# Kernel tuning notes

Hardware: AMD Instinct MI355X
Metric: run time of the kernel (lower is better)

The kernel has to match this reference:

```python
import jax, jax.numpy as jnp
import numpy as np

N = 20000      # nodes per type
E = 320000     # edges per relation
F = 512        # raw feature dim
H = 4          # attention heads
C = 128        # hidden_channels per head
B = 64         # batch_size (num graphs)
HH = H * C
INNER = 64
NEG_SLOPE = 0.2


def _gatv2(x_src, x_dst, ei, Wl, Wr, att, b):
    """PyG GATv2Conv (concat=True, add_self_loops=True, neg_slope=0.2).
    x_src:[Ns,Fin] x_dst:[Nd,Fin'] ei:[2,E] Wl,Wr:[Fin,H*C] att:[H,C] b:[H*C].
    Returns [Nd, H*C]. Self-loop edges appended (inputs assumed loop-free)."""
    n_dst = x_dst.shape[0]
    loop = jnp.arange(min(x_src.shape[0], n_dst), dtype=ei.dtype)
    src = jnp.concatenate([ei[0], loop])
    dst = jnp.concatenate([ei[1], loop])
    xl = (x_src @ Wl).reshape(-1, H, C)   # source-side transform
    xr = (x_dst @ Wr).reshape(-1, H, C)   # target-side transform
    e = jax.nn.leaky_relu(xl[src] + xr[dst], NEG_SLOPE)   # [E',H,C]
    logit = jnp.einsum('ehc,hc->eh', e, att)               # [E',H]
    m = jax.ops.segment_max(logit, dst, num_segments=n_dst)
    m = jnp.where(jnp.isfinite(m), m, 0.0)
    p = jnp.exp(logit - m[dst])
    s = jax.ops.segment_sum(p, dst, num_segments=n_dst)
    alpha = p / jnp.maximum(s[dst], 1e-16)                 # per-dst softmax
    out = jax.ops.segment_sum(alpha[:, :, None] * xl[src], dst, num_segments=n_dst)
    return out.reshape(n_dst, HH) + b


def _layer(x_i, x_j, ei_ii, ei_jj, ei_ij, ei_ji, Wl, Wr, att, b):
    # relation order: 0:(x_i->x_i) 1:(x_j->x_j) 2:(x_i->x_j) 3:(x_j->x_i); HeteroConv aggr='sum'
    oi = _gatv2(x_i, x_i, ei_ii, Wl[0], Wr[0], att[0], b[0]) \
       + _gatv2(x_j, x_i, ei_ji, Wl[3], Wr[3], att[3], b[3])
    oj = _gatv2(x_j, x_j, ei_jj, Wl[1], Wr[1], att[1], b[1]) \
       + _gatv2(x_i, x_j, ei_ij, Wl[2], Wr[2], att[2], b[2])
    # head-sum + tanh: x.view(-1, heads, hidden).sum(1).tanh()
    oi = jnp.tanh(oi.reshape(-1, H, C).sum(axis=1))
    oj = jnp.tanh(oj.reshape(-1, H, C).sum(axis=1))
    return oi, oj


def setup_inputs() -> dict:
    key = jax.random.key(0)
    ks = jax.random.split(key, 24)
    inp = {
        'x_i': jax.random.normal(ks[0], (N, F), jnp.float32),
        'x_j': jax.random.normal(ks[1], (N, F), jnp.float32),
        'ei_ii': jax.random.randint(ks[2], (2, E), 0, N, jnp.int32),
        'ei_jj': jax.random.randint(ks[3], (2, E), 0, N, jnp.int32),
        'ei_ij': jax.random.randint(ks[4], (2, E), 0, N, jnp.int32),
        'ei_ji': jax.random.randint(ks[5], (2, E), 0, N, jnp.int32),
        'batch_i': jnp.sort(jax.random.randint(ks[6], (N,), 0, B, jnp.int32)),
        'batch_j': jnp.sort(jax.random.randint(ks[7], (N,), 0, B, jnp.int32)),
        'Wl0': jax.random.normal(ks[8], (4, F, HH), jnp.float32) / np.sqrt(F),
        'Wr0': jax.random.normal(ks[9], (4, F, HH), jnp.float32) / np.sqrt(F),
        'att0': jax.random.normal(ks[10], (4, H, C), jnp.float32) / np.sqrt(C),
        'b0': jnp.zeros((4, HH), jnp.float32),
        'Wl1': jax.random.normal(ks[11], (4, C, HH), jnp.float32) / np.sqrt(C),
        'Wr1': jax.random.normal(ks[12], (4, C, HH), jnp.float32) / np.sqrt(C),
        'att1': jax.random.normal(ks[13], (4, H, C), jnp.float32) / np.sqrt(C),
        'b1': jnp.zeros((4, HH), jnp.float32),
        'W_out': jax.random.normal(ks[14], (C, 1), jnp.float32) / np.sqrt(C),
        'b_out': jnp.zeros((1,), jnp.float32),
        'W_i': jax.random.normal(ks[15], (C, INNER), jnp.float32) / np.sqrt(C),
        'b_i': jnp.zeros((INNER,), jnp.float32),
        'W_j': jax.random.normal(ks[16], (C, INNER), jnp.float32) / np.sqrt(C),
        'b_j': jnp.zeros((INNER,), jnp.float32),
    }
    return inp


def reference(x_i, x_j, ei_ii, ei_jj, ei_ij, ei_ji, batch_i, batch_j,
              Wl0, Wr0, att0, b0, Wl1, Wr1, att1, b1,
              W_out, b_out, W_i, b_i, W_j, b_j):
    x_i, x_j = _layer(x_i, x_j, ei_ii, ei_jj, ei_ij, ei_ji, Wl0, Wr0, att0, b0)
    x_i, x_j = _layer(x_i, x_j, ei_ii, ei_jj, ei_ij, ei_ji, Wl1, Wr1, att1, b1)
    # global_add_pool per graph, then unsqueeze(1) + tanh
    p_i = jnp.tanh(jax.ops.segment_sum(x_i, batch_i, num_segments=B))[:, None, :]  # [B,1,C]
    p_j = jnp.tanh(jax.ops.segment_sum(x_j, batch_j, num_segments=B))[:, None, :]
    y_i = p_i @ W_i + b_i   # [B,1,INNER]
    y_j = p_j @ W_j + b_j
    x = (p_i + p_j)[:, 0, :]            # cat along dim=1 then sum(dim=1)
    logits = jax.nn.sigmoid(x @ W_out + b_out)   # [B,1]
    return (logits, y_i, y_j)
```

## Files before the change

kernel.cpp:

```cpp
#include <hip/hip_runtime.h>

#define NN      20000
#define EE      320000
#define ETOT    340000
#define FD      512
#define HH_     4
#define CD      128
#define HHD     512
#define BG      64
#define INNERD  64

typedef __attribute__((ext_vector_type(8))) short bf16x8;
typedef __attribute__((ext_vector_type(4))) float f32x4;

__device__ __forceinline__ float bf2f(unsigned v) { return __uint_as_float(v << 16); }
__device__ __forceinline__ unsigned short f2bf(float f) {
    unsigned u = __float_as_uint(f);
    unsigned r = 0x7fffu + ((u >> 16) & 1u);
    return (unsigned short)((u + r) >> 16);
}
__device__ __forceinline__ void load8bf(const unsigned short* p, float* f) {
    uint4 u = *reinterpret_cast<const uint4*>(p);
    f[0] = bf2f(u.x & 0xffffu); f[1] = bf2f(u.x >> 16);
    f[2] = bf2f(u.y & 0xffffu); f[3] = bf2f(u.y >> 16);
    f[4] = bf2f(u.z & 0xffffu); f[5] = bf2f(u.z >> 16);
// ... 56 lines not shown
    if (idx < EE) { src = ei[idx]; dst = ei[EE + idx]; }
    else          { src = dst = idx - EE; }
    int pos = atomicAdd(&cursor[dst], 1);
    srcs[pos] = (unsigned short)src;
}

__global__ __launch_bounds__(256) void csr_hist4(
    const int* __restrict__ e0, const int* __restrict__ e1,
    const int* __restrict__ e2, const int* __restrict__ e3,
    int* __restrict__ cnt)
{
    int idx = blockIdx.x * blockDim.x + threadIdx.x;
    if (idx >= 4 * EE) return;
    int r = idx / EE, e = idx - r * EE;
    const int* ei = r == 0 ? e0 : r == 1 ? e1 : r == 2 ? e2 : e3;
    atomicAdd(&cnt[r * NN + ei[EE + e]], 1);
}

__global__ __launch_bounds__(1024) void csr_scan4(const int* __restrict__ cnt_all,
                                                  int* __restrict__ rowptr_all,
                                                  int* __restrict__ cursor_all)
{
    const int r = blockIdx.x;
    const int* cnt = cnt_all + r * NN;
    int* rowptr = rowptr_all + r * (NN + 4);
    int* cursor = cursor_all + r * NN;
    __shared__ int part[1024];
    int t = threadIdx.x;
    int base = t * 20;
    int s = 0;
    #pragma unroll
    for (int i = 0; i < 20; ++i) { int n = base + i; if (n < NN) s += cnt[n] + 1; }
    part[t] = s;
    __syncthreads();
    for (int off = 1; off < 1024; off <<= 1) {
        int v = (t >= off) ? part[t - off] : 0;
        __syncthreads();
        part[t] += v;
        __syncthreads();
    }
    int run = (t > 0) ? part[t - 1] : 0;
    #pragma unroll
    for (int i = 0; i < 20; ++i) {
        int n = base + i;
        if (n < NN) { rowptr[n] = run; cursor[n] = run; run += cnt[n] + 1; }
    }
    if (t == 1023) rowptr[NN] = run;
}

__global__ __launch_bounds__(256) void csr_scatter4(
    const int* __restrict__ e0, const int* __restrict__ e1,
    const int* __restrict__ e2, const int* __restrict__ e3,
    int* __restrict__ cursor_all, unsigned short* __restrict__ srcs_all)
{
    int idx = blockIdx.x * blockDim.x + threadIdx.x;
    if (idx >= 4 * ETOT) return;
    int r = idx / ETOT, t = idx - r * ETOT;
    const int* ei = r == 0 ? e0 : r == 1 ? e1 : r == 2 ? e2 : e3;
    int src, dst;
    if (t < EE) { src = ei[t]; dst = ei[EE + t]; }
    else        { src = dst = t - EE; }
    int pos = atomicAdd(&cursor_all[r * NN + dst], 1);
    srcs_all[(size_t)r * ETOT + pos] = (unsigned short)src;
}

__device__ __forceinline__ void wsplit_body(const float* __restrict__ W,
                                            unsigned short* __restrict__ Whi,
                                            unsigned short* __restrict__ Wlo,
                                            int K, int bid)
{
    __shared__ float tile[64][65];
    const int nt = 512 / 64;
    int in = bid % nt; int ik = (bid / nt) % (K / 64); int r = bid / (nt * (K / 64));
    int t = threadIdx.x;
    const float* Wr_ = W + (size_t)r * K * 512;
    #pragma unroll
    for (int rep = 0; rep < 16; ++rep) {
// ... 407 lines not shown
    if (k < e) {
        int s0 = sr[k];
        float A0[8];
        load8bf(xl + (size_t)s0 * HHD + lane * 8, A0);
        float d0 = quad_reduce(edge_logit(A0, br, ta));
        float p0 = __expf(d0);
        den += p0;
        #pragma unroll
        for (int j = 0; j < 8; ++j) n[j] += p0 * A0[j];
    }
}

__device__ __forceinline__ void gat_rel(
    const int* __restrict__ rp, const unsigned short* __restrict__ sr,
    const unsigned short* __restrict__ xl, const unsigned short* __restrict__ xr,
    const float* __restrict__ att, int dst, int lane, float* o)
{
    int beg = rp[dst], end = rp[dst + 1];
    float br[8], ta[8];
    load8bf(xr + (size_t)dst * HHD + lane * 8, br);
    #pragma unroll
    for (int j = 0; j < 8; ++j) ta[j] = att[lane * 8 + j];
    float n[8] = {}; float den = 0.f;
    gat_drain(sr, xl, br, ta, beg, end, n, den, lane);
    float inv = 1.f / den;
    #pragma unroll
    for (int j = 0; j < 8; ++j) {
        o[j] = n[j] * inv;
        o[j] += __shfl_xor(o[j], 16);
        o[j] += __shfl_xor(o[j], 32);
    }
}

__device__ __forceinline__ void gat_rel2(
    const int* __restrict__ rp0, const unsigned short* __restrict__ sr0,
    const unsigned short* __restrict__ xl0, const unsigned short* __restrict__ xr0,
    const float* __restrict__ attA,
    const int* __restrict__ rp1, const unsigned short* __restrict__ sr1,
    const unsigned short* __restrict__ xl1, const unsigned short* __restrict__ xr1,
    const float* __restrict__ attB,
    int dst, int lane, float* o0, float* o1)
{
    int k0 = rp0[dst], e0 = rp0[dst + 1];
    int k1 = rp1[dst], e1 = rp1[dst + 1];
    float br0[8], br1[8], ta0[8], ta1[8];
    load8bf(xr0 + (size_t)dst * HHD + lane * 8, br0);
    load8bf(xr1 + (size_t)dst * HHD + lane * 8, br1);
    #pragma unroll
    for (int j = 0; j < 8; ++j) { ta0[j] = attA[lane * 8 + j]; ta1[j] = attB[lane * 8 + j]; }

    float n0[8] = {}, n1[8] = {};
    float den0 = 0.f, den1 = 0.f;

    while (k0 + 2 <= e0 && k1 + 2 <= e1) {
        int sa0 = sr0[k0], sa1 = sr0[k0 + 1];
        int sb0 = sr1[k1], sb1 = sr1[k1 + 1];
        float A0[8], A1[8], B0[8], B1[8];
        load8bf(xl0 + (size_t)sa0 * HHD + lane * 8, A0);
        load8bf(xl0 + (size_t)sa1 * HHD + lane * 8, A1);
// ... 23 lines not shown
    gat_drain(sr1, xl1, br1, ta1, k1, e1, n1, den1, lane);

    float i0 = 1.f / den0, i1 = 1.f / den1;
    #pragma unroll
    for (int j = 0; j < 8; ++j) {
        o0[j] = n0[j] * i0;
        o0[j] += __shfl_xor(o0[j], 16);
        o0[j] += __shfl_xor(o0[j], 32);
        o1[j] = n1[j] * i1;
        o1[j] += __shfl_xor(o1[j], 16);
        o1[j] += __shfl_xor(o1[j], 32);
    }
}

__device__ __forceinline__ void aggr4d_body(
    int dst, int lane,
    const int* __restrict__ rp0, const unsigned short* __restrict__ sr0,
    const unsigned short* __restrict__ xl0, const unsigned short* __restrict__ xr0,
    const float* __restrict__ attA,
    const int* __restrict__ rp1, const unsigned short* __restrict__ sr1,
    const unsigned short* __restrict__ xl1, const unsigned short* __restrict__ xr1,
    const float* __restrict__ attB,
    float* __restrict__ acc, int fin_mode,
    const float* __restrict__ bA, const float* __restrict__ bB,
    unsigned short* __restrict__ z)
{
    float o0[8], o1[8];
    gat_rel2(rp0, sr0, xl0, xr0, attA, rp1, sr1, xl1, xr1, attB, dst, lane, o0, o1);
    #pragma unroll
    for (int j = 0; j < 8; ++j) o1[j] += o0[j];

    if (lane < 16) {
        size_t ai = (size_t)dst * CD + lane * 8;
        int c0 = lane * 8;
        #pragma unroll
        for (int j = 0; j < 8; ++j) {
            float bb = 0.f;
            #pragma unroll
            for (int h = 0; h < HH_; ++h)
                bb += bA[h * CD + c0 + j] + bB[h * CD + c0 + j];
            o1[j] = tanhf(o1[j] + bb);
        }
        if (fin_mode == 1) {
            #pragma unroll
            for (int j = 0; j < 8; ++j) z[ai + j] = f2bf(o1[j]);
        } else {
            #pragma unroll
            for (int j = 0; j < 8; ++j) acc[ai + j] = o1[j];
        }
    }
}

__global__ __launch_bounds__(256) void fused_aggr4(
    const int* __restrict__ rowptr, const unsigned short* __restrict__ srcs,
    const unsigned short* __restrict__ xl, const unsigned short* __restrict__ xr,
    const float* __restrict__ att,
    float* __restrict__ acc, int add_in, int fin_mode,
    const float* __restrict__ bA, const float* __restrict__ bB,
    unsigned short* __restrict__ z,
    const int* __restrict__ batch, float* __restrict__ pool)
{
    int dst = (int)((blockIdx.x * (size_t)blockDim.x + threadIdx.x) >> 6);
    int lane = threadIdx.x & 63;
    if (dst >= NN) return;

    float o[8];
    gat_rel(rowptr, srcs, xl, xr, att, dst, lane, o);

    if (lane < 16) {
        size_t ai = (size_t)dst * CD + lane * 8;
        if (add_in) {
            #pragma unroll
            for (int j = 0; j < 8; ++j) o[j] += acc[ai + j];
        }
        if (fin_mode == 0) {
            #pragma unroll
            for (int j = 0; j < 8; ++j) acc[ai + j] = o[j];
        } else {
            int c0 = lane * 8;
            #pragma unroll
            for (int j = 0; j < 8; ++j) {
                float bb = 0.f;
// ... 8 lines not shown
            } else {
                #pragma unroll
                for (int j = 0; j < 8; ++j) acc[ai + j] = o[j];
            }
        }
    }
}

__global__ __launch_bounds__(256) void fused_aggr4d(
    const int* __restrict__ rp0, const unsigned short* __restrict__ sr0,
    const unsigned short* __restrict__ xl0, const unsigned short* __restrict__ xr0,
    const float* __restrict__ attA,
    const int* __restrict__ rp1, const unsigned short* __restrict__ sr1,
    const unsigned short* __restrict__ xl1, const unsigned short* __restrict__ xr1,
    const float* __restrict__ attB,
    float* __restrict__ acc, int fin_mode,
    const float* __restrict__ bA, const float* __restrict__ bB,
    unsigned short* __restrict__ z,
    const int* __restrict__ batch, float* __restrict__ pool)
{
    int dst = (int)((blockIdx.x * (size_t)blockDim.x + threadIdx.x) >> 6);
    int lane = threadIdx.x & 63;
    if (dst >= NN) return;
    aggr4d_body(dst, lane, rp0, sr0, xl0, xr0, attA, rp1, sr1, xl1, xr1, attB,
                acc, fin_mode, bA, bB, z);
}

__global__ __launch_bounds__(256) void fused_aggr4d_pair(
    const int* __restrict__ irp0, const unsigned short* __restrict__ isr0,
    const unsigned short* __restrict__ ixl0, const unsigned short* __restrict__ ixr0,
    const float* __restrict__ iattA,
    const int* __restrict__ irp1, const unsigned short* __restrict__ isr1,
    const unsigned short* __restrict__ ixl1, const unsigned short* __restrict__ ixr1,
    const float* __restrict__ iattB,
    float* __restrict__ accA,
    const float* __restrict__ ibA, const float* __restrict__ ibB,
    const int* __restrict__ jrp0, const unsigned short* __restrict__ jsr0,
    const unsigned short* __restrict__ jxl0, const unsigned short* __restrict__ jxr0,
    const float* __restrict__ jattA,
    const int* __restrict__ jrp1, const unsigned short* __restrict__ jsr1,
    const unsigned short* __restrict__ jxl1, const unsigned short* __restrict__ jxr1,
    const float* __restrict__ jattB,
    float* __restrict__ accB,
    const float* __restrict__ jbA, const float* __restrict__ jbB)
{
    const int half = NN / 4;
    int lane = threadIdx.x & 63;
    if ((int)blockIdx.x < half) {
        int dst = (int)((blockIdx.x * (size_t)blockDim.x + threadIdx.x) >> 6);
        if (dst >= NN) return;
        aggr4d_body(dst, lane, irp0, isr0, ixl0, ixr0, iattA,
                    irp1, isr1, ixl1, ixr1, iattB, accA, 2, ibA, ibB, nullptr);
    } else {
        int dst = (int)(((blockIdx.x - half) * (size_t)blockDim.x + threadIdx.x) >> 6);
        if (dst >= NN) return;
        aggr4d_body(dst, lane, jrp0, jsr0, jxl0, jxr0, jattA,
                    jrp1, jsr1, jxl1, jxr1, jattB, accB, 2, jbA, jbB, nullptr);
    }
}

template <typename TA, bool A_EXACT>
__global__ __launch_bounds__(256, 3) void gemm_aggr_fused(
    int ngemm, int ntot,
    const TA* __restrict__ A0, const TA* __restrict__ A1,
    const TA* __restrict__ A2, const TA* __restrict__ A3,
    const unsigned short* __restrict__ B0h, const unsigned short* __restrict__ B0l,
    const unsigned short* __restrict__ B1h, const unsigned short* __restrict__ B1l,
    const unsigned short* __restrict__ B2h, const unsigned short* __restrict__ B2l,
    const unsigned short* __restrict__ B3h, const unsigned short* __restrict__ B3l,
    unsigned short* __restrict__ C0, unsigned short* __restrict__ C1,
    unsigned short* __restrict__ C2, unsigned short* __restrict__ C3,
    int M, int K, int N,
    const int* __restrict__ rp0, const unsigned short* __restrict__ sr0,
    const unsigned short* __restrict__ xl0, const unsigned short* __restrict__ xr0,
    const float* __restrict__ attA,
    const int* __restrict__ rp1, const unsigned short* __restrict__ sr1,
    const unsigned short* __restrict__ xl1, const unsigned short* __restrict__ xr1,
    const float* __restrict__ attB,
    float* __restrict__ acc, int fin_mode,
    const float* __restrict__ bA, const float* __restrict__ bB,
    unsigned short* __restrict__ zout)
{
    int b = (int)blockIdx.x;
    int cb = (int)(((long long)b * ngemm) / ntot);
    bool is_gemm = ((int)(((long long)(b + 1) * ngemm) / ntot) > cb);
    if (is_gemm) {
        int g = cb;
        int xcd = g & 7, q8 = ngemm >> 3, r8 = ngemm & 7;
        int work = (xcd < r8 ? xcd * (q8 + 1) : r8 * (q8 + 1) + (xcd - r8) * q8) + (g >> 3);
        const int gx = N / 128, gy = (M + 127) / 128;
        int bx = work % gx; int t2 = work / gx; int by = t2 % gy; int bz = t2 / gy;
        const TA* A = bz == 0 ? A0 : bz == 1 ? A1 : bz == 2 ? A2 : A3;
        const unsigned short* Bh = bz == 0 ? B0h : bz == 1 ? B1h : bz == 2 ? B2h : B3h;
        const unsigned short* Bl = bz == 0 ? B0l : bz == 1 ? B1l : bz == 2 ? B2l : B3l;
        unsigned short* C = bz == 0 ? C0 : bz == 1 ? C1 : bz == 2 ? C2 : C3;
        gemm_body<TA, A_EXACT>(A, Bh, Bl, C, bx, by, M, K, N);
    } else {
        int ab = b - cb;
        int dst = (int)(((size_t)ab * blockDim.x + threadIdx.x) >> 6);
        int lane = threadIdx.x & 63;
        if (dst >= NN) return;
        aggr4d_body(dst, lane, rp0, sr0, xl0, xr0, attA, rp1, sr1, xl1, xr1, attB,
                    acc, fin_mode, bA, bB, zout);
    }
}

__global__ __launch_bounds__(512) void pool_reduce(
    const float* __restrict__ acc, const int* __restrict__ batch,
    float* __restrict__ pool)
{
    int b = blockIdx.x;
    int t = threadIdx.x & (CD - 1);
    int q = threadIdx.x >> 7;
    int lo, hi;
    { int l = 0, r = NN; while (l < r) { int m = (l + r) >> 1; if (batch[m] < b) l = m + 1; else r = m; } lo = l; }
    { int l = lo, r = NN; while (l < r) { int m = (l + r) >> 1; if (batch[m] <= b) l = m + 1; else r = m; } hi = l; }
    float s = 0.f;
// ... 88 lines not shown
                            const float* att, const float* bias, int fin_mode,
                            unsigned short* zout, const int* batch, float* pool,
                            const Ws& w, hipStream_t stream)
{
    dim3 gg(HHD / 128, (NN + 127) / 128, 4);
    size_t off0 = (size_t)rids[0] * HHD * K;
    size_t off1 = (size_t)rids[1] * HHD * K;
    gemm_mfma_t4<TA, A_EXACT><<<gg, 256, 0, stream>>>(
        srcA[0], dstA[0], srcA[1], dstA[1],
        WTl_h + off0, WTl_l + off0, WTr_h + off0, WTr_l + off0,
        WTl_h + off1, WTl_l + off1, WTr_h + off1, WTr_l + off1,
        w.xl, w.xr, w.xl2, w.xr2, NN, K, HHD);
    fused_aggr4d<<<NN / 4, 256, 0, stream>>>(
        rp[0], sr[0], w.xl, w.xr, att + (size_t)rids[0] * HHD,
        rp[1], sr[1], w.xl2, w.xr2, att + (size_t)rids[1] * HHD,
        w.acc, fin_mode,
        bias + (size_t)rids[0] * HHD, bias + (size_t)rids[1] * HHD,
        zout, batch, pool);
}

template <typename TA, bool A_EXACT>
static void run_group_fat_t(const TA* srcA[2], const TA* dstA[2],
                            const int* rp[2], const unsigned short* sr[2],
                            const int rids[2], int K,
                            const unsigned short* WTl_h, const unsigned short* WTl_l,
                            const unsigned short* WTr_h, const unsigned short* WTr_l,
                            const float* att, const float* bias, int fin_mode,
                            unsigned short* zout, const int* batch, float* pool,
                            const Ws& w, hipStream_t stream)
{
    dim3 gg(HHD / 128, (NN + 127) / 128, 2);
    const int ablocks = NN / 4;
    for (int q = 0; q < 2; ++q) {
        int r = rids[q];
        size_t off = (size_t)r * HHD * K;
        gemm_mfma_t<TA, A_EXACT><<<gg, 256, 0, stream>>>(
            srcA[q], dstA[q],
            WTl_h + off, WTl_l + off, WTr_h + off, WTr_l + off,
            w.xl, w.xr, NN, K, HHD);
        int fm = (q == 1) ? fin_mode : 0;
        fused_aggr4<<<ablocks, 256, 0, stream>>>(
            rp[q], sr[q], w.xl, w.xr,
            att + (size_t)r * HHD,
            w.acc, q > 0 ? 1 : 0, fm,
            bias + (size_t)rids[0] * HHD, bias + (size_t)rids[1] * HHD,
            zout, batch, pool);
    }
}

template <typename TA, bool A_EXACT>
static void run_group_fat(const TA* srcA[2], const TA* dstA[2],
                          const int* rp[2], const unsigned short* sr[2],
                          const int rids[2], int K,
                          const float* Wl, const float* Wr, const float* att,
                          const float* bias, int fin_mode,
                          unsigned short* zout, const int* batch, float* pool,
                          const Ws& w, hipStream_t stream)
{
    dim3 gg(HHD / 64, (NN + 63) / 64, 2);
    const int ablocks = NN / 4;
    for (int q = 0; q < 2; ++q) {
        int r = rids[q];
        gemm_mfma<TA, A_EXACT><<<gg, 256, 0, stream>>>(
            srcA[q], dstA[q],
            Wl + (size_t)r * K * HHD, Wr + (size_t)r * K * HHD, HHD,
            w.xl, w.xr, NN, K, HHD);
        int fm = (q == 1) ? fin_mode : 0;
        fused_aggr4<<<ablocks, 256, 0, stream>>>(
            rp[q], sr[q], w.xl, w.xr,
            att + (size_t)r * HHD,
            w.acc, q > 0 ? 1 : 0, fm,
            bias + (size_t)rids[0] * HHD, bias + (size_t)rids[1] * HHD,
            zout, batch, pool);
    }
}

template <typename TA, bool A_EXACT>
static void run_group_thin(const TA* srcA[2], const TA* dstA[2],
                           const int* eis[2], const int rids[2], int K,
                           const float* Wl, const float* Wr, const float* att,
                           const float* bias, int fin_mode,
                           unsigned short* zout, const int* batch, float* pool,
                           const Ws& w, hipStream_t stream)
{
    dim3 gg(2, (NN + 63) / 64, 2);
    const int ablocks = NN / 4;
// ... 35 lines not shown
    const float* b0    = (const float*)d_in[11];
    const float* Wl1   = (const float*)d_in[12];
    const float* Wr1   = (const float*)d_in[13];
    const float* att1  = (const float*)d_in[14];
    const float* b1    = (const float*)d_in[15];
    const float* W_out = (const float*)d_in[16];
    const float* b_out = (const float*)d_in[17];
    const float* W_i   = (const float*)d_in[18];
    const float* b_i   = (const float*)d_in[19];
    const float* W_j   = (const float*)d_in[20];
    const float* b_j   = (const float*)d_in[21];
    float* out = (float*)d_out;

    const size_t FAT2_BYTES = (size_t)NN * HHD * 2 * 2 + (size_t)NN * CD * 4
                            + (size_t)NN * CD * 2 * 2 + 4 * (size_t)ETOT * 2
                            + 4 * (size_t)(NN + 4) * 4 + 4 * (size_t)NN * 4 * 2
                            + (size_t)BG * CD * 4 * 2;
    const size_t FAT1_BYTES = (size_t)NN * HHD * 2 * 2 + (size_t)NN * CD * 4
                            + (size_t)NN * CD * 2 * 2 + (size_t)ETOT * 2
                            + (size_t)(NN + 4) * 4 + (size_t)NN * 4 * 2
                            + (size_t)BG * CD * 4 * 2;
    const size_t WT0_ONE = (size_t)4 * 512 * 512 * 2;
    const size_t WT1_ONE = (size_t)4 * 512 * 128 * 2;
    const size_t WT_BYTES = 4 * WT0_ONE + 4 * WT1_ONE;
    const size_t X2_BYTES = 2 * (size_t)NN * HHD * 2;
    const size_t ACC2_BYTES = (size_t)NN * CD * 4;

    const int ncsr = (ws_size >= FAT2_BYTES) ? 4 : 1;
    const bool fat = (ws_size >= FAT1_BYTES);
    const bool fat_t = (ws_size >= FAT2_BYTES + WT_BYTES);
    const bool fat_m = (ws_size >= FAT2_BYTES + WT_BYTES + X2_BYTES);
    const bool fat_f = (ws_size >= FAT2_BYTES + WT_BYTES + 3 * X2_BYTES);
    const bool fat_g = (ws_size >= FAT2_BYTES + WT_BYTES + 3 * X2_BYTES + ACC2_BYTES);

    Ws w;
    char* p = (char*)d_ws;
    size_t xbytes = fat ? (size_t)NN * HHD * 2 : (size_t)NN * CD * 2;
    w.xl     = (unsigned short*)p; p += xbytes;
    w.xr     = (unsigned short*)p; p += xbytes;
    w.acc    = (float*)p;          p += (size_t)NN * CD * 4;
    w.z_i    = (unsigned short*)p; p += (size_t)NN * CD * 2;
    w.z_j    = (unsigned short*)p; p += (size_t)NN * CD * 2;
    {
        int* rowptr_all = (int*)p;            p += (size_t)ncsr * (NN + 4) * 4;
        unsigned short* srcs_all = (unsigned short*)p; p += (size_t)ncsr * ETOT * 2;
        for (int r = 0; r < 4; ++r) {
            int rr = (r < ncsr) ? r : 0;
            w.rowptr[r] = rowptr_all + (size_t)rr * (NN + 4);
            w.srcs[r]   = srcs_all + (size_t)rr * ETOT;
        }
    }
    w.cnt    = (int*)p;            p += (size_t)ncsr * NN * 4;
    w.cursor = (int*)p;            p += (size_t)ncsr * NN * 4;
    w.pool_i = (float*)p;          p += (size_t)BG * CD * 4;
    w.pool_j = (float*)p;          p += (size_t)BG * CD * 4;
    if (fat_t) {
        w.wt0l_h = (unsigned short*)p; p += WT0_ONE;
        w.wt0l_l = (unsigned short*)p; p += WT0_ONE;
        w.wt0r_h = (unsigned short*)p; p += WT0_ONE;
        w.wt0r_l = (unsigned short*)p; p += WT0_ONE;
        w.wt1l_h = (unsigned short*)p; p += WT1_ONE;
        w.wt1l_l = (unsigned short*)p; p += WT1_ONE;
        w.wt1r_h = (unsigned short*)p; p += WT1_ONE;
        w.wt1r_l = (unsigned short*)p; p += WT1_ONE;
    }
    if (fat_m) {
        w.xl2 = (unsigned short*)p; p += (size_t)NN * HHD * 2;
        w.xr2 = (unsigned short*)p; p += (size_t)NN * HHD * 2;
// ... 12 lines not shown
        hipMemsetAsync(w.pool_i, 0, (size_t)BG * CD * sizeof(float), stream);
        hipMemsetAsync(w.pool_j, 0, (size_t)BG * CD * sizeof(float), stream);
    }

    const int* eis_all[4] = { ei_ii, ei_jj, ei_ij, ei_ji };
    const float* srcA0_i[2] = { x_i, x_j };  const float* dstA0_i[2] = { x_i, x_i };
    const float* srcA0_j[2] = { x_j, x_i };  const float* dstA0_j[2] = { x_j, x_j };
    const int rids_i[2] = { 0, 3 };
    const int rids_j[2] = { 1, 2 };
    const unsigned short* srcA1_i[2] = { w.z_i, w.z_j };
    const unsigned short* dstA1_i[2] = { w.z_i, w.z_i };
    const unsigned short* srcA1_j[2] = { w.z_j, w.z_i };
    const unsigned short* dstA1_j[2] = { w.z_j, w.z_j };

    if (fat_t) {
        hipMemsetAsync(w.cnt, 0, 4 * NN * sizeof(int), stream);
        csr_hist4<<<(4 * EE + 255) / 256, 256, 0, stream>>>(
            ei_ii, ei_jj, ei_ij, ei_ji, w.cnt);
        csr_scan4<<<4, 1024, 0, stream>>>(w.cnt, w.rowptr[0], w.cursor);
        csr_scatter4<<<(4 * ETOT + 255) / 256, 256, 0, stream>>>(
            ei_ii, ei_jj, ei_ij, ei_ji, w.cursor, w.srcs[0]);
        wsplit_all<<<640, 256, 0, stream>>>(
            Wl0, Wr0, Wl1, Wr1,
            w.wt0l_h, w.wt0l_l, w.wt0r_h, w.wt0r_l,
            w.wt1l_h, w.wt1l_l, w.wt1r_h, w.wt1r_l);

        const int* rp_i[2] = { w.rowptr[0], w.rowptr[3] };
        const unsigned short* sr_i[2] = { w.srcs[0], w.srcs[3] };
        const int* rp_j[2] = { w.rowptr[1], w.rowptr[2] };
        const unsigned short* sr_j[2] = { w.srcs[1], w.srcs[2] };

        if (fat_g) {
            const size_t o0 = (size_t)0 * HHD * FD, o3 = (size_t)3 * HHD * FD;
            const size_t o1 = (size_t)1 * HHD * FD, o2 = (size_t)2 * HHD * FD;
            const size_t p0 = (size_t)0 * HHD * CD, p1 = (size_t)1 * HHD * CD;
            const size_t p2 = (size_t)2 * HHD * CD, p3 = (size_t)3 * HHD * CD;
            dim3 gg(HHD / 128, (NN + 127) / 128, 4);
            gemm_mfma_t4<float, false><<<gg, 256, 0, stream>>>(
                x_i, x_i, x_j, x_i,
                w.wt0l_h + o0, w.wt0l_l + o0, w.wt0r_h + o0, w.wt0r_l + o0,
                w.wt0l_h + o3, w.wt0l_l + o3, w.wt0r_h + o3, w.wt0r_l + o3,
                w.xl, w.xr, w.xl2, w.xr2, NN, FD, HHD);
            const int ngemm0 = (HHD / 128) * ((NN + 127) / 128) * 4;
            const int ntot0 = ngemm0 + NN / 4;
            gemm_aggr_fused<float, false><<<ntot0, 256, 0, stream>>>(
                ngemm0, ntot0,
                x_j, x_j, x_i, x_j,
                w.wt0l_h + o1, w.wt0l_l + o1, w.wt0r_h + o1, w.wt0r_l + o1,
                w.wt0l_h + o2, w.wt0l_l + o2, w.wt0r_h + o2, w.wt0r_l + o2,
                w.xl3, w.xr3, w.xl4, w.xr4, NN, FD, HHD,
                w.rowptr[0], w.srcs[0], w.xl, w.xr, att0 + (size_t)0 * HHD,
                w.rowptr[3], w.srcs[3], w.xl2, w.xr2, att0 + (size_t)3 * HHD,
                w.acc, 1, b0 + (size_t)0 * HHD, b0 + (size_t)3 * HHD, w.z_i);
            gemm_aggr_fused<unsigned short, true><<<ntot0, 256, 0, stream>>>(
                ngemm0, ntot0,
                w.z_i, w.z_i, w.z_i, w.z_i,
                w.wt1l_h + p0, w.wt1l_l + p0, w.wt1r_h + p0, w.wt1r_l + p0,
                w.wt1r_h + p3, w.wt1r_l + p3, w.wt1l_h + p2, w.wt1l_l + p2,
                w.xl, w.xr, w.xr2, w.xl2, NN, CD, HHD,
                w.rowptr[1], w.srcs[1], w.xl3, w.xr3, att0 + (size_t)1 * HHD,
                w.rowptr[2], w.srcs[2], w.xl4, w.xr4, att0 + (size_t)2 * HHD,
                w.acc, 1, b0 + (size_t)1 * HHD, b0 + (size_t)2 * HHD, w.z_j);
            gemm_mfma_t4<unsigned short, true><<<gg, 256, 0, stream>>>(
                w.z_j, w.z_j, w.z_j, w.z_j,
                w.wt1l_h + p3, w.wt1l_l + p3, w.wt1l_h + p1, w.wt1l_l + p1,
                w.wt1r_h + p1, w.wt1r_l + p1, w.wt1r_h + p2, w.wt1r_l + p2,
                w.xl4, w.xl3, w.xr3, w.xr4, NN, CD, HHD);
            fused_aggr4d_pair<<<2 * (NN / 4), 256, 0, stream>>>(
                w.rowptr[0], w.srcs[0], w.xl, w.xr, att1 + (size_t)0 * HHD,
                w.rowptr[3], w.srcs[3], w.xl4, w.xr2, att1 + (size_t)3 * HHD,
                w.acc, b1 + (size_t)0 * HHD, b1 + (size_t)3 * HHD,
                w.rowptr[1], w.srcs[1], w.xl3, w.xr3, att1 + (size_t)1 * HHD,
                w.rowptr[2], w.srcs[2], w.xl2, w.xr4, att1 + (size_t)2 * HHD,
                w.acc2, b1 + (size_t)1 * HHD, b1 + (size_t)2 * HHD);
            pool_reduce2<<<2 * BG, 512, 0, stream>>>(
                w.acc, batch_i, w.pool_i, w.acc2, batch_j, w.pool_j);
        } else if (fat_f) {
            const size_t o0 = (size_t)0 * HHD * FD, o3 = (size_t)3 * HHD * FD;
            const size_t o1 = (size_t)1 * HHD * FD, o2 = (size_t)2 * HHD * FD;
            dim3 gg(HHD / 128, (NN + 127) / 128, 4);
            gemm_mfma_t4<float, false><<<gg, 256, 0, stream>>>(
                x_i, x_i, x_j, x_i,
                w.wt0l_h + o0, w.wt0l_l + o0, w.wt0r_h + o0, w.wt0r_l + o0,
                w.wt0l_h + o3, w.wt0l_l + o3, w.wt0r_h + o3, w.wt0r_l + o3,
                w.xl, w.xr, w.xl2, w.xr2, NN, FD, HHD);
            const int ngemm = (HHD / 128) * ((NN + 127) / 128) * 4;
            const int ntot = ngemm + NN / 4;
            gemm_aggr_fused<float, false><<<ntot, 256, 0, stream>>>(
                ngemm, ntot,
                x_j, x_j, x_i, x_j,
                w.wt0l_h + o1, w.wt0l_l + o1, w.wt0r_h + o1, w.wt0r_l + o1,
                w.wt0l_h + o2, w.wt0l_l + o2, w.wt0r_h + o2, w.wt0r_l + o2,
                w.xl3, w.xr3, w.xl4, w.xr4, NN, FD, HHD,
                w.rowptr[0], w.srcs[0], w.xl, w.xr, att0 + (size_t)0 * HHD,
                w.rowptr[3], w.srcs[3], w.xl2, w.xr2, att0 + (size_t)3 * HHD,
                w.acc, 1, b0 + (size_t)0 * HHD, b0 + (size_t)3 * HHD, w.z_i);
            fused_aggr4d<<<NN / 4, 256, 0, stream>>>(
                w.rowptr[1], w.srcs[1], w.xl3, w.xr3, att0 + (size_t)1 * HHD,
                w.rowptr[2], w.srcs[2], w.xl4, w.xr4, att0 + (size_t)2 * HHD,
                w.acc, 1, b0 + (size_t)1 * HHD, b0 + (size_t)2 * HHD,
                w.z_j, nullptr, nullptr);
            dim3 g8(HHD / 128, (NN + 127) / 128, 8);
            gemm_mfma_L1x8<<<g8, 256, 0, stream>>>(
                w.z_i, w.z_j, w.wt1l_h, w.wt1l_l, w.wt1r_h, w.wt1r_l,
                w.xl, w.xr, w.xl2, w.xr2, w.xl3, w.xr3, w.xl4, w.xr4,
                NN, CD, HHD);
            fused_aggr4d<<<NN / 4, 256, 0, stream>>>(
                w.rowptr[0], w.srcs[0], w.xl, w.xr, att1 + (size_t)0 * HHD,
                w.rowptr[3], w.srcs[3], w.xl2, w.xr2, att1 + (size_t)3 * HHD,
                w.acc, 2, b1 + (size_t)0 * HHD, b1 + (size_t)3 * HHD,
                nullptr, nullptr, nullptr);
            pool_reduce<<<BG, 512, 0, stream>>>(w.acc, batch_i, w.pool_i);
            fused_aggr4d<<<NN / 4, 256, 0, stream>>>(
                w.rowptr[1], w.srcs[1], w.xl3, w.xr3, att1 + (size_t)1 * HHD,
                w.rowptr[2], w.srcs[2], w.xl4, w.xr4, att1 + (size_t)2 * HHD,
                w.acc, 2, b1 + (size_t)1 * HHD, b1 + (size_t)2 * HHD,
                nullptr, nullptr, nullptr);
            pool_reduce<<<BG, 512, 0, stream>>>(w.acc, batch_j, w.pool_j);
        } else if (fat_m) {
            run_group_fat_m<float, false>(srcA0_i, dstA0_i, rp_i, sr_i, rids_i, FD,
                                          w.wt0l_h, w.wt0l_l, w.wt0r_h, w.wt0r_l,
                                          att0, b0, 1, w.z_i, nullptr, nullptr, w, stream);
            run_group_fat_m<float, false>(srcA0_j, dstA0_j, rp_j, sr_j, rids_j, FD,
                                          w.wt0l_h, w.wt0l_l, w.wt0r_h, w.wt0r_l,
                                          att0, b0, 1, w.z_j, nullptr, nullptr, w, stream);
            run_group_fat_m<unsigned short, true>(srcA1_i, dstA1_i, rp_i, sr_i, rids_i, CD,
                                                  w.wt1l_h, w.wt1l_l, w.wt1r_h, w.wt1r_l,
                                                  att1, b1, 2, nullptr, batch_i, w.pool_i, w, stream);
            pool_reduce<<<BG, 512, 0, stream>>>(w.acc, batch_i, w.pool_i);
            run_group_fat_m<unsigned short, true>(srcA1_j, dstA1_j, rp_j, sr_j, rids_j, CD,
                                                  w.wt1l_h, w.wt1l_l, w.wt1r_h, w.wt1r_l,
// ... 36 lines not shown
        } else {
            for (int pass = 0; pass < 4; ++pass) {
                const int* rids = (pass & 1) ? rids_j : rids_i;
                for (int q = 0; q < 2; ++q) {
                    int r = rids[q];
                    build_csr(eis_all[r], w.rowptr[0], w.srcs[0], w.cnt, w.cursor, stream);
                    dim3 gg(HHD / 64, (NN + 63) / 64, 2);
                    if (pass < 2) {
                        const float* sa = (pass == 0) ? srcA0_i[q] : srcA0_j[q];
                        const float* da = (pass == 0) ? dstA0_i[q] : dstA0_j[q];
                        gemm_mfma<float, false><<<gg, 256, 0, stream>>>(
                            sa, da, Wl0 + (size_t)r * FD * HHD, Wr0 + (size_t)r * FD * HHD,
                            HHD, w.xl, w.xr, NN, FD, HHD);
                        fused_aggr4<<<NN / 4, 256, 0, stream>>>(
                            w.rowptr[0], w.srcs[0], w.xl, w.xr, att0 + (size_t)r * HHD,
                            w.acc, q, (q == 1) ? 1 : 0,
                            b0 + (size_t)rids[0] * HHD, b0 + (size_t)rids[1] * HHD,
                            (pass == 0) ? w.z_i : w.z_j, nullptr, nullptr);
                    } else {
                        const unsigned short* sa = (pass == 2) ? srcA1_i[q] : srcA1_j[q];
                        const unsigned short* da = (pass == 2) ? dstA1_i[q] : dstA1_j[q];
                        gemm_mfma<unsigned short, true><<<gg, 256, 0, stream>>>(
                            sa, da, Wl1 + (size_t)r * CD * HHD, Wr1 + (size_t)r * CD * HHD,
                            HHD, w.xl, w.xr, NN, CD, HHD);
                        fused_aggr4<<<NN / 4, 256, 0, stream>>>(
                            w.rowptr[0], w.srcs[0], w.xl, w.xr, att1 + (size_t)r * HHD,
                            w.acc, q, (q == 1) ? 2 : 0,
                            b1 + (size_t)rids[0] * HHD, b1 + (size_t)rids[1] * HHD,
                            nullptr, (pass == 2) ? batch_i : batch_j,
                            (pass == 2) ? w.pool_i : w.pool_j);
                    }
                }
                if (pass == 2)
                    pool_reduce<<<BG, 512, 0, stream>>>(w.acc, batch_i, w.pool_i);
                else if (pass == 3)
                    pool_reduce<<<BG, 512, 0, stream>>>(w.acc, batch_j, w.pool_j);
            }
        }
    } else {
        const int* eis_i[2] = { ei_ii, ei_ji };
        const int* eis_j[2] = { ei_jj, ei_ij };
        run_group_thin<float, false>(srcA0_i, dstA0_i, eis_i, rids_i, FD, Wl0, Wr0, att0, b0,
// ... 13 lines not shown
```

Before: 1.249 ms.

## Bucket CSR neighbor lists by source range for gather locality

CSR construction now keys each row on destination plus one of eight source-index buckets, so every destination's neighbor list comes out roughly sorted by source. Aggregation kernels read row bounds with a stride to span all buckets of a destination. The aim is more locality and cache reuse in the xl row gathers. In exchange it adds an 8x larger count, cursor and rowptr array and a heavier single-block scan. It also drops the proportional interleaving of GEMM and aggregation blocks in the fused kernel, putting all GEMM blocks first.

```diff
diff --git a/kernel.cpp b/kernel.cpp
--- a/kernel.cpp
+++ b/kernel.cpp
@@ -9,6 +9,8 @@
 #define HHD     512
 #define BG      64
 #define INNERD  64
+#define NBUCK   8
+#define BROWS   (NN * NBUCK)
 
 typedef __attribute__((ext_vector_type(8))) short bf16x8;
 typedef __attribute__((ext_vector_type(4))) float f32x4;
@@ -95,7 +97,8 @@
     if (idx >= 4 * EE) return;
     int r = idx / EE, e = idx - r * EE;
     const int* ei = r == 0 ? e0 : r == 1 ? e1 : r == 2 ? e2 : e3;
-    atomicAdd(&cnt[r * NN + ei[EE + e]], 1);
+    int src = ei[e], dst = ei[EE + e];
+    atomicAdd(&cnt[r * BROWS + dst * NBUCK + src / 2500], 1);
 }
 
 __global__ __launch_bounds__(1024) void csr_scan4(const int* __restrict__ cnt_all,
@@ -103,15 +106,21 @@
                                                   int* __restrict__ cursor_all)
 {
     const int r = blockIdx.x;
-    const int* cnt = cnt_all + r * NN;
-    int* rowptr = rowptr_all + r * (NN + 4);
-    int* cursor = cursor_all + r * NN;
+    const int* cnt = cnt_all + r * BROWS;
+    int* rowptr = rowptr_all + r * (BROWS + 4);
+    int* cursor = cursor_all + r * BROWS;
     __shared__ int part[1024];
     int t = threadIdx.x;
-    int base = t * 20;
+    const int RPT = (BROWS + 1023) / 1024;
+    int base = t * RPT;
     int s = 0;
-    #pragma unroll
-    for (int i = 0; i < 20; ++i) { int n = base + i; if (n < NN) s += cnt[n] + 1; }
+    for (int i = 0; i < RPT; ++i) {
+        int row = base + i;
+        if (row < BROWS) {
+            int dst = row >> 3, bu = row & 7;
+            s += cnt[row] + ((bu == dst / 2500) ? 1 : 0);
+        }
+    }
     part[t] = s;
     __syncthreads();
     for (int off = 1; off < 1024; off <<= 1) {
@@ -121,12 +130,15 @@
         __syncthreads();
     }
     int run = (t > 0) ? part[t - 1] : 0;
-    #pragma unroll
-    for (int i = 0; i < 20; ++i) {
-        int n = base + i;
-        if (n < NN) { rowptr[n] = run; cursor[n] = run; run += cnt[n] + 1; }
-    }
-    if (t == 1023) rowptr[NN] = run;
+    for (int i = 0; i < RPT; ++i) {
+        int row = base + i;
+        if (row < BROWS) {
+            int dst = row >> 3, bu = row & 7;
+            rowptr[row] = run; cursor[row] = run;
+            run += cnt[row] + ((bu == dst / 2500) ? 1 : 0);
+        }
+    }
+    if (t == 1023) rowptr[BROWS] = run;
 }
 
 __global__ __launch_bounds__(256) void csr_scatter4(
@@ -141,7 +153,8 @@
     int src, dst;
     if (t < EE) { src = ei[t]; dst = ei[EE + t]; }
     else        { src = dst = t - EE; }
-    int pos = atomicAdd(&cursor_all[r * NN + dst], 1);
+    int row = r * BROWS + dst * NBUCK + src / 2500;
+    int pos = atomicAdd(&cursor_all[row], 1);
     srcs_all[(size_t)r * ETOT + pos] = (unsigned short)src;
 }
 
@@ -579,9 +592,9 @@
 __device__ __forceinline__ void gat_rel(
     const int* __restrict__ rp, const unsigned short* __restrict__ sr,
     const unsigned short* __restrict__ xl, const unsigned short* __restrict__ xr,
-    const float* __restrict__ att, int dst, int lane, float* o)
-{
-    int beg = rp[dst], end = rp[dst + 1];
+    const float* __restrict__ att, int dst, int lane, int rs, float* o)
+{
+    int beg = rp[dst * rs], end = rp[dst * rs + rs];
     float br[8], ta[8];
     load8bf(xr + (size_t)dst * HHD + lane * 8, br);
     #pragma unroll
@@ -604,10 +617,10 @@
     const int* __restrict__ rp1, const unsigned short* __restrict__ sr1,
     const unsigned short* __restrict__ xl1, const unsigned short* __restrict__ xr1,
     const float* __restrict__ attB,
-    int dst, int lane, float* o0, float* o1)
-{
-    int k0 = rp0[dst], e0 = rp0[dst + 1];
-    int k1 = rp1[dst], e1 = rp1[dst + 1];
+    int dst, int lane, int rs, float* o0, float* o1)
+{
+    int k0 = rp0[dst * rs], e0 = rp0[dst * rs + rs];
+    int k1 = rp1[dst * rs], e1 = rp1[dst * rs + rs];
     float br0[8], br1[8], ta0[8], ta1[8];
     load8bf(xr0 + (size_t)dst * HHD + lane * 8, br0);
     load8bf(xr1 + (size_t)dst * HHD + lane * 8, br1);
@@ -661,7 +674,7 @@
 }
 
 __device__ __forceinline__ void aggr4d_body(
-    int dst, int lane,
+    int dst, int lane, int rs,
     const int* __restrict__ rp0, const unsigned short* __restrict__ sr0,
     const unsigned short* __restrict__ xl0, const unsigned short* __restrict__ xr0,
     const float* __restrict__ attA,
@@ -673,7 +686,7 @@
     unsigned short* __restrict__ z)
 {
     float o0[8], o1[8];
-    gat_rel2(rp0, sr0, xl0, xr0, attA, rp1, sr1, xl1, xr1, attB, dst, lane, o0, o1);
+    gat_rel2(rp0, sr0, xl0, xr0, attA, rp1, sr1, xl1, xr1, attB, dst, lane, rs, o0, o1);
     #pragma unroll
     for (int j = 0; j < 8; ++j) o1[j] += o0[j];
 
@@ -702,7 +715,7 @@
     const int* __restrict__ rowptr, const unsigned short* __restrict__ srcs,
     const unsigned short* __restrict__ xl, const unsigned short* __restrict__ xr,
     const float* __restrict__ att,
-    float* __restrict__ acc, int add_in, int fin_mode,
+    float* __restrict__ acc, int add_in, int fin_mode, int rs,
     const float* __restrict__ bA, const float* __restrict__ bB,
     unsigned short* __restrict__ z,
     const int* __restrict__ batch, float* __restrict__ pool)
@@ -712,7 +725,7 @@
     if (dst >= NN) return;
 
     float o[8];
-    gat_rel(rowptr, srcs, xl, xr, att, dst, lane, o);
+    gat_rel(rowptr, srcs, xl, xr, att, dst, lane, rs, o);
 
     if (lane < 16) {
         size_t ai = (size_t)dst * CD + lane * 8;
@@ -751,7 +764,7 @@
     const int* __restrict__ rp1, const unsigned short* __restrict__ sr1,
     const unsigned short* __restrict__ xl1, const unsigned short* __restrict__ xr1,
     const float* __restrict__ attB,
-    float* __restrict__ acc, int fin_mode,
+    float* __restrict__ acc, int fin_mode, int rs,
     const float* __restrict__ bA, const float* __restrict__ bB,
     unsigned short* __restrict__ z,
     const int* __restrict__ batch, float* __restrict__ pool)
@@ -759,11 +772,12 @@
     int dst = (int)((blockIdx.x * (size_t)blockDim.x + threadIdx.x) >> 6);
     int lane = threadIdx.x & 63;
     if (dst >= NN) return;
-    aggr4d_body(dst, lane, rp0, sr0, xl0, xr0, attA, rp1, sr1, xl1, xr1, attB,
+    aggr4d_body(dst, lane, rs, rp0, sr0, xl0, xr0, attA, rp1, sr1, xl1, xr1, attB,
                 acc, fin_mode, bA, bB, z);
 }
 
 __global__ __launch_bounds__(256) void fused_aggr4d_pair(
+    int rs,
     const int* __restrict__ irp0, const unsigned short* __restrict__ isr0,
     const unsigned short* __restrict__ ixl0, const unsigned short* __restrict__ ixr0,
     const float* __restrict__ iattA,
@@ -786,19 +800,19 @@
     if ((int)blockIdx.x < half) {
         int dst = (int)((blockIdx.x * (size_t)blockDim.x + threadIdx.x) >> 6);
         if (dst >= NN) return;
-        aggr4d_body(dst, lane, irp0, isr0, ixl0, ixr0, iattA,
+        aggr4d_body(dst, lane, rs, irp0, isr0, ixl0, ixr0, iattA,
                     irp1, isr1, ixl1, ixr1, iattB, accA, 2, ibA, ibB, nullptr);
     } else {
         int dst = (int)(((blockIdx.x - half) * (size_t)blockDim.x + threadIdx.x) >> 6);
         if (dst >= NN) return;
-        aggr4d_body(dst, lane, jrp0, jsr0, jxl0, jxr0, jattA,
+        aggr4d_body(dst, lane, rs, jrp0, jsr0, jxl0, jxr0, jattA,
                     jrp1, jsr1, jxl1, jxr1, jattB, accB, 2, jbA, jbB, nullptr);
     }
 }
 
 template <typename TA, bool A_EXACT>
 __global__ __launch_bounds__(256, 3) void gemm_aggr_fused(
-    int ngemm, int ntot,
+    int ngemm, int rs,
     const TA* __restrict__ A0, const TA* __restrict__ A1,
     const TA* __restrict__ A2, const TA* __restrict__ A3,
     const unsigned short* __restrict__ B0h, const unsigned short* __restrict__ B0l,
@@ -818,13 +832,10 @@
     const float* __restrict__ bA, const float* __restrict__ bB,
     unsigned short* __restrict__ zout)
 {
-    int b = (int)blockIdx.x;
-    int cb = (int)(((long long)b * ngemm) / ntot);
-    bool is_gemm = ((int)(((long long)(b + 1) * ngemm) / ntot) > cb);
-    if (is_gemm) {
-        int g = cb;
-        int xcd = g & 7, q8 = ngemm >> 3, r8 = ngemm & 7;
-        int work = (xcd < r8 ? xcd * (q8 + 1) : r8 * (q8 + 1) + (xcd - r8) * q8) + (g >> 3);
+    if ((int)blockIdx.x < ngemm) {
+        int b = blockIdx.x;
+        int xcd = b & 7, q8 = ngemm >> 3, r8 = ngemm & 7;
+        int work = (xcd < r8 ? xcd * (q8 + 1) : r8 * (q8 + 1) + (xcd - r8) * q8) + (b >> 3);
         const int gx = N / 128, gy = (M + 127) / 128;
         int bx = work % gx; int t2 = work / gx; int by = t2 % gy; int bz = t2 / gy;
         const TA* A = bz == 0 ? A0 : bz == 1 ? A1 : bz == 2 ? A2 : A3;
@@ -833,11 +844,10 @@
         unsigned short* C = bz == 0 ? C0 : bz == 1 ? C1 : bz == 2 ? C2 : C3;
         gemm_body<TA, A_EXACT>(A, Bh, Bl, C, bx, by, M, K, N);
     } else {
-        int ab = b - cb;
-        int dst = (int)(((size_t)ab * blockDim.x + threadIdx.x) >> 6);
+        int dst = (int)(((blockIdx.x - ngemm) * (size_t)blockDim.x + threadIdx.x) >> 6);
         int lane = threadIdx.x & 63;
         if (dst >= NN) return;
-        aggr4d_body(dst, lane, rp0, sr0, xl0, xr0, attA, rp1, sr1, xl1, xr1, attB,
+        aggr4d_body(dst, lane, rs, rp0, sr0, xl0, xr0, attA, rp1, sr1, xl1, xr1, attB,
                     acc, fin_mode, bA, bB, zout);
     }
 }
@@ -956,7 +966,7 @@
     fused_aggr4d<<<NN / 4, 256, 0, stream>>>(
         rp[0], sr[0], w.xl, w.xr, att + (size_t)rids[0] * HHD,
         rp[1], sr[1], w.xl2, w.xr2, att + (size_t)rids[1] * HHD,
-        w.acc, fin_mode,
+        w.acc, fin_mode, NBUCK,
         bias + (size_t)rids[0] * HHD, bias + (size_t)rids[1] * HHD,
         zout, batch, pool);
 }
@@ -984,7 +994,7 @@
         fused_aggr4<<<ablocks, 256, 0, stream>>>(
             rp[q], sr[q], w.xl, w.xr,
             att + (size_t)r * HHD,
-            w.acc, q > 0 ? 1 : 0, fm,
+            w.acc, q > 0 ? 1 : 0, fm, NBUCK,
             bias + (size_t)rids[0] * HHD, bias + (size_t)rids[1] * HHD,
             zout, batch, pool);
     }
@@ -1011,7 +1021,7 @@
         fused_aggr4<<<ablocks, 256, 0, stream>>>(
             rp[q], sr[q], w.xl, w.xr,
             att + (size_t)r * HHD,
-            w.acc, q > 0 ? 1 : 0, fm,
+            w.acc, q > 0 ? 1 : 0, fm, 1,
             bias + (size_t)rids[0] * HHD, bias + (size_t)rids[1] * HHD,
             zout, batch, pool);
     }
@@ -1077,7 +1087,7 @@
 
     const size_t FAT2_BYTES = (size_t)NN * HHD * 2 * 2 + (size_t)NN * CD * 4
                             + (size_t)NN * CD * 2 * 2 + 4 * (size_t)ETOT * 2
-                            + 4 * (size_t)(NN + 4) * 4 + 4 * (size_t)NN * 4 * 2
+                            + 4 * (size_t)(BROWS + 4) * 4 + 4 * (size_t)BROWS * 4 * 2
                             + (size_t)BG * CD * 4 * 2;
     const size_t FAT1_BYTES = (size_t)NN * HHD * 2 * 2 + (size_t)NN * CD * 4
                             + (size_t)NN * CD * 2 * 2 + (size_t)ETOT * 2
@@ -1105,16 +1115,16 @@
     w.z_i    = (unsigned short*)p; p += (size_t)NN * CD * 2;
     w.z_j    = (unsigned short*)p; p += (size_t)NN * CD * 2;
     {
-        int* rowptr_all = (int*)p;            p += (size_t)ncsr * (NN + 4) * 4;
+        int* rowptr_all = (int*)p;            p += (size_t)ncsr * (BROWS + 4) * 4;
         unsigned short* srcs_all = (unsigned short*)p; p += (size_t)ncsr * ETOT * 2;
         for (int r = 0; r < 4; ++r) {
             int rr = (r < ncsr) ? r : 0;
-            w.rowptr[r] = rowptr_all + (size_t)rr * (NN + 4);
+            w.rowptr[r] = rowptr_all + (size_t)rr * (BROWS + 4);
             w.srcs[r]   = srcs_all + (size_t)rr * ETOT;
         }
     }
-    w.cnt    = (int*)p;            p += (size_t)ncsr * NN * 4;
-    w.cursor = (int*)p;            p += (size_t)ncsr * NN * 4;
+    w.cnt    = (int*)p;            p += (size_t)ncsr * BROWS * 4;
+    w.cursor = (int*)p;            p += (size_t)ncsr * BROWS * 4;
     w.pool_i = (float*)p;          p += (size_t)BG * CD * 4;
     w.pool_j = (float*)p;          p += (size_t)BG * CD * 4;
     if (fat_t) {
@@ -1157,7 +1167,7 @@
     const unsigned short* dstA1_j[2] = { w.z_j, w.z_j };
 
     if (fat_t) {
-        hipMemsetAsync(w.cnt, 0, 4 * NN * sizeof(int), stream);
+        hipMemsetAsync(w.cnt, 0, 4 * (size_t)BROWS * sizeof(int), stream);
         csr_hist4<<<(4 * EE + 255) / 256, 256, 0, stream>>>(
             ei_ii, ei_jj, ei_ij, ei_ji, w.cnt);
         csr_scan4<<<4, 1024, 0, stream>>>(w.cnt, w.rowptr[0], w.cursor);
@@ -1185,9 +1195,8 @@
                 w.wt0l_h + o3, w.wt0l_l + o3, w.wt0r_h + o3, w.wt0r_l + o3,
                 w.xl, w.xr, w.xl2, w.xr2, NN, FD, HHD);
             const int ngemm0 = (HHD / 128) * ((NN + 127) / 128) * 4;
-            const int ntot0 = ngemm0 + NN / 4;
-            gemm_aggr_fused<float, false><<<ntot0, 256, 0, stream>>>(
-                ngemm0, ntot0,
+            gemm_aggr_fused<float, false><<<ngemm0 + NN / 4, 256, 0, stream>>>(
+                ngemm0, NBUCK,
                 x_j, x_j, x_i, x_j,
                 w.wt0l_h + o1, w.wt0l_l + o1, w.wt0r_h + o1, w.wt0r_l + o1,
                 w.wt0l_h + o2, w.wt0l_l + o2, w.wt0r_h + o2, w.wt0r_l + o2,
@@ -1195,8 +1204,8 @@
                 w.rowptr[0], w.srcs[0], w.xl, w.xr, att0 + (size_t)0 * HHD,
                 w.rowptr[3], w.srcs[3], w.xl2, w.xr2, att0 + (size_t)3 * HHD,
                 w.acc, 1, b0 + (size_t)0 * HHD, b0 + (size_t)3 * HHD, w.z_i);
-            gemm_aggr_fused<unsigned short, true><<<ntot0, 256, 0, stream>>>(
-                ngemm0, ntot0,
+            gemm_aggr_fused<unsigned short, true><<<ngemm0 + NN / 4, 256, 0, stream>>>(
+                ngemm0, NBUCK,
                 w.z_i, w.z_i, w.z_i, w.z_i,
                 w.wt1l_h + p0, w.wt1l_l + p0, w.wt1r_h + p0, w.wt1r_l + p0,
                 w.wt1r_h + p3, w.wt1r_l + p3, w.wt1l_h + p2, w.wt1l_l + p2,
@@ -1210,6 +1219,7 @@
                 w.wt1r_h + p1, w.wt1r_l + p1, w.wt1r_h + p2, w.wt1r_l + p2,
                 w.xl4, w.xl3, w.xr3, w.xr4, NN, CD, HHD);
             fused_aggr4d_pair<<<2 * (NN / 4), 256, 0, stream>>>(
+                NBUCK,
                 w.rowptr[0], w.srcs[0], w.xl, w.xr, att1 + (size_t)0 * HHD,
                 w.rowptr[3], w.srcs[3], w.xl4, w.xr2, att1 + (size_t)3 * HHD,
                 w.acc, b1 + (size_t)0 * HHD, b1 + (size_t)3 * HHD,
@@ -1228,9 +1238,8 @@
                 w.wt0l_h + o3, w.wt0l_l + o3, w.wt0r_h + o3, w.wt0r_l + o3,
                 w.xl, w.xr, w.xl2, w.xr2, NN, FD, HHD);
             const int ngemm = (HHD / 128) * ((NN + 127) / 128) * 4;
-            const int ntot = ngemm + NN / 4;
-            gemm_aggr_fused<float, false><<<ntot, 256, 0, stream>>>(
-                ngemm, ntot,
+            gemm_aggr_fused<float, false><<<ngemm + NN / 4, 256, 0, stream>>>(
+                ngemm, NBUCK,
                 x_j, x_j, x_i, x_j,
                 w.wt0l_h + o1, w.wt0l_l + o1, w.wt0r_h + o1, w.wt0r_l + o1,
                 w.wt0l_h + o2, w.wt0l_l + o2, w.wt0r_h + o2, w.wt0r_l + o2,
@@ -1241,7 +1250,7 @@
             fused_aggr4d<<<NN / 4, 256, 0, stream>>>(
                 w.rowptr[1], w.srcs[1], w.xl3, w.xr3, att0 + (size_t)1 * HHD,
                 w.rowptr[2], w.srcs[2], w.xl4, w.xr4, att0 + (size_t)2 * HHD,
-                w.acc, 1, b0 + (size_t)1 * HHD, b0 + (size_t)2 * HHD,
+                w.acc, 1, NBUCK, b0 + (size_t)1 * HHD, b0 + (size_t)2 * HHD,
                 w.z_j, nullptr, nullptr);
             dim3 g8(HHD / 128, (NN + 127) / 128, 8);
             gemm_mfma_L1x8<<<g8, 256, 0, stream>>>(
@@ -1251,13 +1260,13 @@
             fused_aggr4d<<<NN / 4, 256, 0, stream>>>(
                 w.rowptr[0], w.srcs[0], w.xl, w.xr, att1 + (size_t)0 * HHD,
                 w.rowptr[3], w.srcs[3], w.xl2, w.xr2, att1 + (size_t)3 * HHD,
-                w.acc, 2, b1 + (size_t)0 * HHD, b1 + (size_t)3 * HHD,
+                w.acc, 2, NBUCK, b1 + (size_t)0 * HHD, b1 + (size_t)3 * HHD,
                 nullptr, nullptr, nullptr);
             pool_reduce<<<BG, 512, 0, stream>>>(w.acc, batch_i, w.pool_i);
             fused_aggr4d<<<NN / 4, 256, 0, stream>>>(
                 w.rowptr[1], w.srcs[1], w.xl3, w.xr3, att1 + (size_t)1 * HHD,
                 w.rowptr[2], w.srcs[2], w.xl4, w.xr4, att1 + (size_t)2 * HHD,
-                w.acc, 2, b1 + (size_t)1 * HHD, b1 + (size_t)2 * HHD,
+                w.acc, 2, NBUCK, b1 + (size_t)1 * HHD, b1 + (size_t)2 * HHD,
                 nullptr, nullptr, nullptr);
             pool_reduce<<<BG, 512, 0, stream>>>(w.acc, batch_j, w.pool_j);
         } else if (fat_m) {
@@ -1324,7 +1333,7 @@
                             HHD, w.xl, w.xr, NN, FD, HHD);
                         fused_aggr4<<<NN / 4, 256, 0, stream>>>(
                             w.rowptr[0], w.srcs[0], w.xl, w.xr, att0 + (size_t)r * HHD,
-                            w.acc, q, (q == 1) ? 1 : 0,
+                            w.acc, q, (q == 1) ? 1 : 0, 1,
                             b0 + (size_t)rids[0] * HHD, b0 + (size_t)rids[1] * HHD,
                             (pass == 0) ? w.z_i : w.z_j, nullptr, nullptr);
                     } else {
@@ -1335,7 +1344,7 @@
                             HHD, w.xl, w.xr, NN, CD, HHD);
                         fused_aggr4<<<NN / 4, 256, 0, stream>>>(
                             w.rowptr[0], w.srcs[0], w.xl, w.xr, att1 + (size_t)r * HHD,
-                            w.acc, q, (q == 1) ? 2 : 0,
+                            w.acc, q, (q == 1) ? 2 : 0, 1,
                             b1 + (size_t)rids[0] * HHD, b1 + (size_t)rids[1] * HHD,
                             nullptr, (pass == 2) ? batch_i : batch_j,
                             (pass == 2) ? w.pool_i : w.pool_j);
```

New measurement: 1.603 ms. 28.4% more time.
